# Optimization experiments

Measured on AMD Instinct MI355X. Metric: run time of the kernel, lower is better.

The kernel has to match this reference:

```python
import jax, jax.numpy as jnp
import numpy as np

B, T, OBS, ACT, H, OUT, NLAYERS = 4096, 50, 64, 16, 256, 64, 5


def setup_inputs() -> dict:
    key = jax.random.key(0)
    ks = jax.random.split(key, 8)
    w = 0.05
    return {
        "trajectory": jax.random.normal(ks[0], (B, T, OBS), dtype=jnp.float32),
        "actions": jax.random.normal(ks[1], (B, T, ACT), dtype=jnp.float32),
        "Wi": jax.random.normal(ks[2], (OBS + ACT, 4 * H), dtype=jnp.float32) * w,
        "Wh": jax.random.normal(ks[3], (H, 4 * H), dtype=jnp.float32) * w,
        "bh": jnp.zeros((4 * H,), dtype=jnp.float32),
        "mlp_W": jax.random.normal(ks[4], (NLAYERS, H, H), dtype=jnp.float32) * w,
        "mlp_b": jnp.zeros((NLAYERS, H), dtype=jnp.float32),
        "Wout": jax.random.normal(ks[5], (H, OUT), dtype=jnp.float32) * w,
        "bout": jnp.zeros((OUT,), dtype=jnp.float32),
    }


def reference(trajectory, actions, Wi, Wh, bh, mlp_W, mlp_b, Wout, bout):
    # Features extractor = flatten (identity for 1D sensor obs); preprocess is identity for Box.
    x = jnp.concatenate([trajectory, actions], axis=-1)  # [B, T, OBS+ACT]
    xs = jnp.swapaxes(x, 0, 1)  # [T, B, D] for scan over time

    hdim = Wh.shape[0]
    c0 = jnp.zeros((x.shape[0], hdim), dtype=x.dtype)
    h0 = jnp.zeros((x.shape[0], hdim), dtype=x.dtype)

    def step(carry, xt):
        c, h = carry
        z = xt @ Wi + h @ Wh + bh  # [B, 4H]
        zi, zf, zg, zo = jnp.split(z, 4, axis=-1)
        i = jax.nn.sigmoid(zi)
        f = jax.nn.sigmoid(zf)
        g = jax.nn.silu(zg)  # activation_fn=nn.silu
        o = jax.nn.sigmoid(zo)
        c_new = f * c + i * g
        h_new = o * jax.nn.silu(c_new)
        return (c_new, h_new), None

    (c, h), _ = jax.lax.scan(step, (c0, h0), xs)

    out = h
    for k in range(mlp_W.shape[0]):
        out = jax.nn.silu(out @ mlp_W[k] + mlp_b[k])
    pred = out @ Wout + bout
    return pred
```

## Files before the change

kernel.cpp:

```cpp
#include <hip/hip_runtime.h>
#include <hip/hip_fp16.h>


typedef _Float16 h8 __attribute__((ext_vector_type(8)));
typedef _Float16 hv4 __attribute__((ext_vector_type(4)));
typedef float f4 __attribute__((ext_vector_type(4)));

#define NB    4096
#define TSEQ  50
#define DOBS  64
#define DACT  16
#define HD    256
#define DOUT  64
#define NL    5

#define NKT   11
#define AROW  360
#define MTILE 16
#define NWG   (NB / MTILE)
#define NTHR  512

#define WS_MLP   (704 * 512)
#define WS_WOUT  (WS_MLP + 640 * 512)

#define LDS_AS     (MTILE * AROW)
#define LDS_WCOFF  (2 * LDS_AS)
#define WCB        16
#define LDS_HALVES (LDS_WCOFF + 8 * WCB * 512)
#define LDS_BYTES  (LDS_HALVES * 2)
static_assert(LDS_BYTES <= 160 * 1024, "LDS overflow");

#define SB_P     13
#define NSTREAM  52

__device__ __forceinline__ void lds_barrier() {
  asm volatile("s_waitcnt lgkmcnt(0)\n\ts_barrier" ::: "memory");
}

__device__ constexpr int soff(int c) {
  int kt, cbb, g;
  if (c < 20)      { kt = c >> 2;              cbb = 1; g = c & 3; }
  else if (c < 24) { kt = 5;                   cbb = 0; g = c - 20; }
  else if (c < 28) { kt = 5;                   cbb = 1; g = c - 24; }
  else if (c < 44) { kt = 6 + ((c - 28) >> 2); cbb = 1; g = (c - 28) & 3; }
  else if (c < 48) { kt = 10;                  cbb = 0; g = c - 44; }
  else             { kt = 10;                  cbb = 1; g = c - 48; }
  return ((g * 16 + cbb) * NKT + kt) * 512;
}

__global__ void __launch_bounds__(256) repack_kernel(
    const float* __restrict__ Wi, const float* __restrict__ Wh,
    const float* __restrict__ mlpW, const float* __restrict__ Wout,
    _Float16* __restrict__ wsW)
{
  const int gt  = blockIdx.x * 256 + threadIdx.x;
  const int gb  = gt >> 6;
  const int l   = gt & 63;
  const int l15 = l & 15;
  const int kb  = (l >> 4) * 8;
  h8 v;
  if (gb < 704) {
    const int nt = gb / NKT, kt = gb - nt * NKT;
    const int n  = nt * 16 + l15;
#pragma unroll
    for (int j = 0; j < 8; ++j) {
      const int k = kt * 32 + kb + j;
      float s = 0.f;
      if (k < 80)       s = Wi[k * 1024 + n];
      else if (k < 336) s = Wh[(k - 80) * 1024 + n];
      v[j] = (_Float16)s;
    }
  } else if (gb < 1344) {
    const int b2 = gb - 704;
    const int L  = b2 >> 7, rr = b2 & 127;
    const int nt = rr >> 3, kt = rr & 7;
    const int n  = nt * 16 + l15;
#pragma unroll
    for (int j = 0; j < 8; ++j) {
      const int k = kt * 32 + kb + j;
      v[j] = (_Float16)mlpW[(size_t)L * 65536 + k * 256 + n];
    }
  } else {
    const int b3 = gb - 1344;
    const int nt = b3 >> 3, kt = b3 & 7;
    const int n  = nt * 16 + l15;
#pragma unroll
    for (int j = 0; j < 8; ++j) {
      const int k = kt * 32 + kb + j;
      v[j] = (_Float16)Wout[k * 64 + n];
    }
  }
  *(h8*)&wsW[(size_t)gb * 512 + l * 8] = v;
}

__global__ void __launch_bounds__(NTHR, 2) lstm_kernel(
    const float* __restrict__ traj, const float* __restrict__ acts,
    const float* __restrict__ bh,   const float* __restrict__ mlpb,
    const float* __restrict__ bout, const _Float16* __restrict__ wsW,
    float* __restrict__ out)
{
  extern __shared__ __align__(16) _Float16 lds[];
  _Float16* As0 = lds;
  _Float16* As1 = lds + LDS_AS;
  _Float16* Wc  = lds + LDS_WCOFF;

  const int tid = threadIdx.x;
  const int w   = tid >> 6;
  const int l   = tid & 63;
  const int l15 = l & 15;
  const int lq  = l >> 4;
  const int rbase = blockIdx.x * MTILE;

  for (int i = tid; i < 2 * LDS_AS; i += NTHR) lds[i] = (_Float16)0.f;

#pragma unroll
  for (int j = 0; j < WCB; ++j) {
    const int g = j & 3, kt = 6 + (j >> 2);
    const h8 v = *(const h8*)&wsW[(size_t)((g * 16 + w * 2) * NKT + kt) * 512 + l * 8];
    *(h8*)&Wc[(w * WCB + j) * 512 + l * 8] = v;
  }

  h8 rw[20];
#pragma unroll
  for (int kt = 0; kt < 5; ++kt)
#pragma unroll
    for (int g = 0; g < 4; ++g)
      rw[kt * 4 + g] = *(const h8*)&wsW[(size_t)((g * 16 + w * 2) * NKT + kt) * 512 + l * 8];

  float c[2][4];
#pragma unroll
  for (int cb = 0; cb < 2; ++cb)
#pragma unroll
    for (int r = 0; r < 4; ++r) c[cb][r] = 0.f;

  float bias[4][2];
#pragma unroll
  for (int g = 0; g < 4; ++g) {
    bias[g][0] = bh[g * 256 + w * 32 + l15];
    bias[g][1] = bh[g * 256 + w * 32 + 16 + l15];
  }

  __syncthreads();

  if (tid < 256) {
    const int r = tid >> 4, q = tid & 15;
    const float4 v = *(const float4*)&traj[(size_t)(rbase + r) * (TSEQ * DOBS) + q * 4];
    hv4 hx = { (_Float16)v.x, (_Float16)v.y, (_Float16)v.z, (_Float16)v.w };
    *(hv4*)&As0[r * AROW + q * 4] = hx;
  } else {
    const int r = (tid - 256) >> 4, q = (tid - 256) & 15;
    As0[r * AROW + 64 + q] = (_Float16)acts[(size_t)(rbase + r) * (TSEQ * DACT) + q];
  }
  __syncthreads();

  unsigned long long wbits = (unsigned long long)(const void*)wsW;

  h8 sb[SB_P];
  {
    const _Float16* wlb0 = wsW + (size_t)(w * 2 * NKT) * 512 + l * 8;
#pragma unroll
    for (int cc = 0; cc < SB_P; ++cc) sb[cc] = *(const h8*)&wlb0[soff(cc)];
  }

  auto step = [&](int t, const _Float16* buf, _Float16* nbuf) {
    asm volatile("" : "+s"(wbits) : : "memory");
    const _Float16* wst = (const _Float16*)wbits;
    const _Float16* wlb = wst + (size_t)(w * 2 * NKT) * 512 + l * 8;

    float4 xv; float xa;
    const bool havex = (t + 1 < TSEQ);
    if (havex) {
      if (tid < 256) {
        const int r = tid >> 4, q = tid & 15;
        xv = *(const float4*)&traj[(size_t)(rbase + r) * (TSEQ * DOBS) + (t + 1) * DOBS + q * 4];
      } else {
        const int r = (tid - 256) >> 4, q = (tid - 256) & 15;
        xa = acts[(size_t)(rbase + r) * (TSEQ * DACT) + (t + 1) * DACT + q];
      }
    }

    f4 acc0[4], acc1[4];
#pragma unroll
    for (int g = 0; g < 4; ++g) {
      acc0[g] = f4{0.f, 0.f, 0.f, 0.f};
      acc1[g] = f4{0.f, 0.f, 0.f, 0.f};
    }

#pragma unroll
    for (int kt = 0; kt < NKT; ++kt) {
      const h8 a0 = *(const h8*)&buf[l15 * AROW + kt * 32 + lq * 8];
#pragma unroll
      for (int g = 0; g < 4; ++g) {
        if (kt < 5) {
          acc0[g] = __builtin_amdgcn_mfma_f32_16x16x32_f16(a0, rw[kt * 4 + g], acc0[g], 0, 0, 0);
        } else if (kt >= 6 && kt <= 9) {
          const h8 bf0 = *(const h8*)&Wc[(w * WCB + (kt - 6) * 4 + g) * 512 + l * 8];
          acc0[g] = __builtin_amdgcn_mfma_f32_16x16x32_f16(a0, bf0, acc0[g], 0, 0, 0);
        } else {
          const int c0 = (kt == 5) ? (20 + g) : (44 + g);
          acc0[g] = __builtin_amdgcn_mfma_f32_16x16x32_f16(a0, sb[c0 % SB_P], acc0[g], 0, 0, 0);
          sb[c0 % SB_P] = *(const h8*)&wlb[soff((c0 + SB_P) % NSTREAM)];
        }

        const int c1 = kt * 4 + g + (kt >= 5 ? 4 : 0) + (kt >= 10 ? 4 : 0);
        acc1[g] = __builtin_amdgcn_mfma_f32_16x16x32_f16(a0, sb[c1 % SB_P], acc1[g], 0, 0, 0);
        sb[c1 % SB_P] = *(const h8*)&wlb[soff((c1 + SB_P) % NSTREAM)];
      }
    }

    const float KE = -1.44269504088896f;
    {
      const int colh = 80 + w * 32 + l15;
#pragma unroll
      for (int r = 0; r < 4; ++r) {
        const float zi = acc0[0][r] + bias[0][0];
        const float zf = acc0[1][r] + bias[1][0];
        const float zg = acc0[2][r] + bias[2][0];
        const float zo = acc0[3][r] + bias[3][0];
        const float ei = __builtin_amdgcn_exp2f(zi * KE);
        const float ef = __builtin_amdgcn_exp2f(zf * KE);
        const float eg = __builtin_amdgcn_exp2f(zg * KE);
        const float eo = __builtin_amdgcn_exp2f(zo * KE);
        const float fg = __builtin_amdgcn_rcpf(1.f + ef);
        const float igg = zg * __builtin_amdgcn_rcpf((1.f + ei) * (1.f + eg));
        const float cn = fg * c[0][r] + igg;
        c[0][r] = cn;
        const float ec = __builtin_amdgcn_exp2f(cn * KE);
        const float hn = cn * __builtin_amdgcn_rcpf((1.f + eo) * (1.f + ec));
        nbuf[(lq * 4 + r) * AROW + colh] = (_Float16)hn;
      }
    }
    {
      const int colh = 80 + w * 32 + 16 + l15;
#pragma unroll
      for (int r = 0; r < 4; ++r) {
        const float zi = acc1[0][r] + bias[0][1];
        const float zf = acc1[1][r] + bias[1][1];
        const float zg = acc1[2][r] + bias[2][1];
        const float zo = acc1[3][r] + bias[3][1];
        const float ei = __builtin_amdgcn_exp2f(zi * KE);
        const float ef = __builtin_amdgcn_exp2f(zf * KE);
        const float eg = __builtin_amdgcn_exp2f(zg * KE);
        const float eo = __builtin_amdgcn_exp2f(zo * KE);
        const float fg = __builtin_amdgcn_rcpf(1.f + ef);
        const float igg = zg * __builtin_amdgcn_rcpf((1.f + ei) * (1.f + eg));
        const float cn = fg * c[1][r] + igg;
        c[1][r] = cn;
        const float ec = __builtin_amdgcn_exp2f(cn * KE);
        const float hn = cn * __builtin_amdgcn_rcpf((1.f + eo) * (1.f + ec));
        nbuf[(lq * 4 + r) * AROW + colh] = (_Float16)hn;
      }
    }

    if (havex) {
      if (tid < 256) {
        const int r = tid >> 4, q = tid & 15;
        hv4 hx = { (_Float16)xv.x, (_Float16)xv.y, (_Float16)xv.z, (_Float16)xv.w };
        *(hv4*)&nbuf[r * AROW + q * 4] = hx;
      } else {
        const int r = (tid - 256) >> 4, q = (tid - 256) & 15;
        nbuf[r * AROW + 64 + q] = (_Float16)xa;
      }
    }
  };

#pragma unroll 1
  for (int t = 0; t < TSEQ; t += 2) {
    step(t, As0, As1);
    lds_barrier();
    step(t + 1, As1, As0);
    lds_barrier();
  }

  for (int i = tid; i < MTILE * HD; i += NTHR) {
    const int r = i >> 8, cc = i & 255;
    As1[r * AROW + cc] = As0[r * AROW + 80 + cc];
  }
  __syncthreads();

#pragma unroll 1
  for (int L = 0; L < NL; ++L) {
    const _Float16* in = (L & 1) ? As0 : As1;
    _Float16*       ob = (L & 1) ? As1 : As0;
    const _Float16* wl = wsW + WS_MLP + (size_t)L * (128 * 512);
    float bcol[2];
    bcol[0] = mlpb[L * HD + w * 32 + l15];
    bcol[1] = mlpb[L * HD + w * 32 + 16 + l15];

    f4 acc[2];
    acc[0] = f4{0.f, 0.f, 0.f, 0.f};
    acc[1] = f4{0.f, 0.f, 0.f, 0.f};
#pragma unroll
    for (int kt = 0; kt < 8; ++kt) {
      const h8 a0 = *(const h8*)&in[l15 * AROW + kt * 32 + lq * 8];
#pragma unroll
      for (int cb = 0; cb < 2; ++cb) {
        const h8 bf = *(const h8*)&wl[(size_t)((w * 2 + cb) * 8 + kt) * 512 + l * 8];
        acc[cb] = __builtin_amdgcn_mfma_f32_16x16x32_f16(a0, bf, acc[cb], 0, 0, 0);
      }
    }
#pragma unroll
    for (int cb = 0; cb < 2; ++cb)
#pragma unroll
      for (int r = 0; r < 4; ++r) {
        const float z = acc[cb][r] + bcol[cb];
        const float ez = __builtin_amdgcn_exp2f(z * -1.44269504088896f);
        ob[(lq * 4 + r) * AROW + w * 32 + cb * 16 + l15] =
            (_Float16)(z * __builtin_amdgcn_rcpf(1.f + ez));
      }
    __syncthreads();
  }

  if (w < 4) {
    const _Float16* wo = wsW + WS_WOUT;
    const float bo = bout[w * 16 + l15];
    f4 acc0 = f4{0.f, 0.f, 0.f, 0.f};
#pragma unroll
    for (int kt = 0; kt < 8; ++kt) {
      const h8 a0 = *(const h8*)&As0[l15 * AROW + kt * 32 + lq * 8];
      const h8 bf = *(const h8*)&wo[(size_t)(w * 8 + kt) * 512 + l * 8];
      acc0 = __builtin_amdgcn_mfma_f32_16x16x32_f16(a0, bf, acc0, 0, 0, 0);
    }
#pragma unroll
    for (int r = 0; r < 4; ++r)
      out[(size_t)(rbase + lq * 4 + r) * DOUT + w * 16 + l15] = acc0[r] + bo;
  }
}

extern "C" void kernel_launch(void* const* d_in, const int* in_sizes, int n_in,
                              void* d_out, int out_size, void* d_ws, size_t ws_size,
                              hipStream_t stream)
{
  const float* traj = (const float*)d_in[0];
  const float* acts = (const float*)d_in[1];
  const float* Wi   = (const float*)d_in[2];
  const float* Wh   = (const float*)d_in[3];
  const float* bh   = (const float*)d_in[4];
  const float* mlpW = (const float*)d_in[5];
  const float* mlpb = (const float*)d_in[6];
  const float* Wout = (const float*)d_in[7];
  const float* bout = (const float*)d_in[8];
  _Float16* wsW = (_Float16*)d_ws;

  (void)hipFuncSetAttribute((const void*)lstm_kernel,
                            hipFuncAttributeMaxDynamicSharedMemorySize, LDS_BYTES);

  repack_kernel<<<344, 256, 0, stream>>>(Wi, Wh, mlpW, Wout, wsW);
  lstm_kernel<<<NWG, NTHR, LDS_BYTES, stream>>>(traj, acts, bh, mlpb, bout, wsW, (float*)d_out);
}
```

Before: 335.0 us.

## Split LSTM gate columns across 16 waves instead of 8 per workgroup

Doubles the workgroup to 1024 threads so each wave owns 16 hidden columns, not 32. This halves the serial MFMA chain per wave in each recurrent timestep. Weight residency is rebalanced to fit: K-tiles 0-2 in registers, 3-4 in LDS, 5-10 streamed from global with a shorter prefetch ring. Total LDS use is about the same, but more waves now compete for register and global bandwidth.

```diff
diff --git a/kernel.cpp b/kernel.cpp
--- a/kernel.cpp
+++ b/kernel.cpp
@@ -18,34 +18,27 @@
 #define AROW  360
 #define MTILE 16
 #define NWG   (NB / MTILE)
-#define NTHR  512
+#define NTHR  1024
 
 #define WS_MLP   (704 * 512)
 #define WS_WOUT  (WS_MLP + 640 * 512)
 
 #define LDS_AS     (MTILE * AROW)
 #define LDS_WCOFF  (2 * LDS_AS)
-#define WCB        16
-#define LDS_HALVES (LDS_WCOFF + 8 * WCB * 512)
+#define WCB        8
+#define LDS_HALVES (LDS_WCOFF + 16 * WCB * 512)
 #define LDS_BYTES  (LDS_HALVES * 2)
 static_assert(LDS_BYTES <= 160 * 1024, "LDS overflow");
 
-#define SB_P     13
-#define NSTREAM  52
+#define SB_P     6
+#define NSTREAM  24
 
 __device__ __forceinline__ void lds_barrier() {
   asm volatile("s_waitcnt lgkmcnt(0)\n\ts_barrier" ::: "memory");
 }
 
 __device__ constexpr int soff(int c) {
-  int kt, cbb, g;
-  if (c < 20)      { kt = c >> 2;              cbb = 1; g = c & 3; }
-  else if (c < 24) { kt = 5;                   cbb = 0; g = c - 20; }
-  else if (c < 28) { kt = 5;                   cbb = 1; g = c - 24; }
-  else if (c < 44) { kt = 6 + ((c - 28) >> 2); cbb = 1; g = (c - 28) & 3; }
-  else if (c < 48) { kt = 10;                  cbb = 0; g = c - 44; }
-  else             { kt = 10;                  cbb = 1; g = c - 48; }
-  return ((g * 16 + cbb) * NKT + kt) * 512;
+  return (((c & 3) * 16) * NKT + 5 + (c >> 2)) * 512;
 }
 
 __global__ void __launch_bounds__(256) repack_kernel(
@@ -93,7 +86,7 @@
   *(h8*)&wsW[(size_t)gb * 512 + l * 8] = v;
 }
 
-__global__ void __launch_bounds__(NTHR, 2) lstm_kernel(
+__global__ void __launch_bounds__(NTHR, 4) lstm_kernel(
     const float* __restrict__ traj, const float* __restrict__ acts,
     const float* __restrict__ bh,   const float* __restrict__ mlpb,
     const float* __restrict__ bout, const _Float16* __restrict__ wsW,
@@ -115,30 +108,25 @@
 
 #pragma unroll
   for (int j = 0; j < WCB; ++j) {
-    const int g = j & 3, kt = 6 + (j >> 2);
-    const h8 v = *(const h8*)&wsW[(size_t)((g * 16 + w * 2) * NKT + kt) * 512 + l * 8];
+    const int g = j & 3, kt = 3 + (j >> 2);
+    const h8 v = *(const h8*)&wsW[(size_t)((g * 16 + w) * NKT + kt) * 512 + l * 8];
     *(h8*)&Wc[(w * WCB + j) * 512 + l * 8] = v;
   }
 
-  h8 rw[20];
-#pragma unroll
-  for (int kt = 0; kt < 5; ++kt)
+  h8 rw[12];
+#pragma unroll
+  for (int kt = 0; kt < 3; ++kt)
 #pragma unroll
     for (int g = 0; g < 4; ++g)
-      rw[kt * 4 + g] = *(const h8*)&wsW[(size_t)((g * 16 + w * 2) * NKT + kt) * 512 + l * 8];
-
-  float c[2][4];
-#pragma unroll
-  for (int cb = 0; cb < 2; ++cb)
-#pragma unroll
-    for (int r = 0; r < 4; ++r) c[cb][r] = 0.f;
-
-  float bias[4][2];
-#pragma unroll
-  for (int g = 0; g < 4; ++g) {
-    bias[g][0] = bh[g * 256 + w * 32 + l15];
-    bias[g][1] = bh[g * 256 + w * 32 + 16 + l15];
-  }
+      rw[kt * 4 + g] = *(const h8*)&wsW[(size_t)((g * 16 + w) * NKT + kt) * 512 + l * 8];
+
+  float c[4];
+#pragma unroll
+  for (int r = 0; r < 4; ++r) c[r] = 0.f;
+
+  float bias[4];
+#pragma unroll
+  for (int g = 0; g < 4; ++g) bias[g] = bh[g * 256 + w * 16 + l15];
 
   __syncthreads();
 
@@ -147,7 +135,7 @@
     const float4 v = *(const float4*)&traj[(size_t)(rbase + r) * (TSEQ * DOBS) + q * 4];
     hv4 hx = { (_Float16)v.x, (_Float16)v.y, (_Float16)v.z, (_Float16)v.w };
     *(hv4*)&As0[r * AROW + q * 4] = hx;
-  } else {
+  } else if (tid < 512) {
     const int r = (tid - 256) >> 4, q = (tid - 256) & 15;
     As0[r * AROW + 64 + q] = (_Float16)acts[(size_t)(rbase + r) * (TSEQ * DACT) + q];
   }
@@ -157,7 +145,7 @@
 
   h8 sb[SB_P];
   {
-    const _Float16* wlb0 = wsW + (size_t)(w * 2 * NKT) * 512 + l * 8;
+    const _Float16* wlb0 = wsW + (size_t)(w * NKT) * 512 + l * 8;
 #pragma unroll
     for (int cc = 0; cc < SB_P; ++cc) sb[cc] = *(const h8*)&wlb0[soff(cc)];
   }
@@ -165,7 +153,7 @@
   auto step = [&](int t, const _Float16* buf, _Float16* nbuf) {
     asm volatile("" : "+s"(wbits) : : "memory");
     const _Float16* wst = (const _Float16*)wbits;
-    const _Float16* wlb = wst + (size_t)(w * 2 * NKT) * 512 + l * 8;
+    const _Float16* wlb = wst + (size_t)(w * NKT) * 512 + l * 8;
 
     float4 xv; float xa;
     const bool havex = (t + 1 < TSEQ);
@@ -173,79 +161,51 @@
       if (tid < 256) {
         const int r = tid >> 4, q = tid & 15;
         xv = *(const float4*)&traj[(size_t)(rbase + r) * (TSEQ * DOBS) + (t + 1) * DOBS + q * 4];
-      } else {
+      } else if (tid < 512) {
         const int r = (tid - 256) >> 4, q = (tid - 256) & 15;
         xa = acts[(size_t)(rbase + r) * (TSEQ * DACT) + (t + 1) * DACT + q];
       }
     }
 
-    f4 acc0[4], acc1[4];
-#pragma unroll
-    for (int g = 0; g < 4; ++g) {
-      acc0[g] = f4{0.f, 0.f, 0.f, 0.f};
-      acc1[g] = f4{0.f, 0.f, 0.f, 0.f};
-    }
+    f4 acc[4];
+#pragma unroll
+    for (int g = 0; g < 4; ++g) acc[g] = f4{0.f, 0.f, 0.f, 0.f};
 
 #pragma unroll
     for (int kt = 0; kt < NKT; ++kt) {
       const h8 a0 = *(const h8*)&buf[l15 * AROW + kt * 32 + lq * 8];
 #pragma unroll
       for (int g = 0; g < 4; ++g) {
-        if (kt < 5) {
-          acc0[g] = __builtin_amdgcn_mfma_f32_16x16x32_f16(a0, rw[kt * 4 + g], acc0[g], 0, 0, 0);
-        } else if (kt >= 6 && kt <= 9) {
-          const h8 bf0 = *(const h8*)&Wc[(w * WCB + (kt - 6) * 4 + g) * 512 + l * 8];
-          acc0[g] = __builtin_amdgcn_mfma_f32_16x16x32_f16(a0, bf0, acc0[g], 0, 0, 0);
+        if (kt < 3) {
+          acc[g] = __builtin_amdgcn_mfma_f32_16x16x32_f16(a0, rw[kt * 4 + g], acc[g], 0, 0, 0);
+        } else if (kt < 5) {
+          const h8 bf = *(const h8*)&Wc[(w * WCB + (kt - 3) * 4 + g) * 512 + l * 8];
+          acc[g] = __builtin_amdgcn_mfma_f32_16x16x32_f16(a0, bf, acc[g], 0, 0, 0);
         } else {
-          const int c0 = (kt == 5) ? (20 + g) : (44 + g);
-          acc0[g] = __builtin_amdgcn_mfma_f32_16x16x32_f16(a0, sb[c0 % SB_P], acc0[g], 0, 0, 0);
-          sb[c0 % SB_P] = *(const h8*)&wlb[soff((c0 + SB_P) % NSTREAM)];
+          const int cc = (kt - 5) * 4 + g;
+          acc[g] = __builtin_amdgcn_mfma_f32_16x16x32_f16(a0, sb[cc % SB_P], acc[g], 0, 0, 0);
+          sb[cc % SB_P] = *(const h8*)&wlb[soff((cc + SB_P) % NSTREAM)];
         }
-
-        const int c1 = kt * 4 + g + (kt >= 5 ? 4 : 0) + (kt >= 10 ? 4 : 0);
-        acc1[g] = __builtin_amdgcn_mfma_f32_16x16x32_f16(a0, sb[c1 % SB_P], acc1[g], 0, 0, 0);
-        sb[c1 % SB_P] = *(const h8*)&wlb[soff((c1 + SB_P) % NSTREAM)];
       }
     }
 
     const float KE = -1.44269504088896f;
     {
-      const int colh = 80 + w * 32 + l15;
+      const int colh = 80 + w * 16 + l15;
 #pragma unroll
       for (int r = 0; r < 4; ++r) {
-        const float zi = acc0[0][r] + bias[0][0];
-        const float zf = acc0[1][r] + bias[1][0];
-        const float zg = acc0[2][r] + bias[2][0];
-        const float zo = acc0[3][r] + bias[3][0];
+        const float zi = acc[0][r] + bias[0];
+        const float zf = acc[1][r] + bias[1];
+        const float zg = acc[2][r] + bias[2];
+        const float zo = acc[3][r] + bias[3];
         const float ei = __builtin_amdgcn_exp2f(zi * KE);
         const float ef = __builtin_amdgcn_exp2f(zf * KE);
         const float eg = __builtin_amdgcn_exp2f(zg * KE);
         const float eo = __builtin_amdgcn_exp2f(zo * KE);
         const float fg = __builtin_amdgcn_rcpf(1.f + ef);
         const float igg = zg * __builtin_amdgcn_rcpf((1.f + ei) * (1.f + eg));
-        const float cn = fg * c[0][r] + igg;
-        c[0][r] = cn;
-        const float ec = __builtin_amdgcn_exp2f(cn * KE);
-        const float hn = cn * __builtin_amdgcn_rcpf((1.f + eo) * (1.f + ec));
-        nbuf[(lq * 4 + r) * AROW + colh] = (_Float16)hn;
-      }
-    }
-    {
-      const int colh = 80 + w * 32 + 16 + l15;
-#pragma unroll
-      for (int r = 0; r < 4; ++r) {
-        const float zi = acc1[0][r] + bias[0][1];
-        const float zf = acc1[1][r] + bias[1][1];
-        const float zg = acc1[2][r] + bias[2][1];
-        const float zo = acc1[3][r] + bias[3][1];
-        const float ei = __builtin_amdgcn_exp2f(zi * KE);
-        const float ef = __builtin_amdgcn_exp2f(zf * KE);
-        const float eg = __builtin_amdgcn_exp2f(zg * KE);
-        const float eo = __builtin_amdgcn_exp2f(zo * KE);
-        const float fg = __builtin_amdgcn_rcpf(1.f + ef);
-        const float igg = zg * __builtin_amdgcn_rcpf((1.f + ei) * (1.f + eg));
-        const float cn = fg * c[1][r] + igg;
-        c[1][r] = cn;
+        const float cn = fg * c[r] + igg;
+        c[r] = cn;
         const float ec = __builtin_amdgcn_exp2f(cn * KE);
         const float hn = cn * __builtin_amdgcn_rcpf((1.f + eo) * (1.f + ec));
         nbuf[(lq * 4 + r) * AROW + colh] = (_Float16)hn;
@@ -257,7 +217,7 @@
         const int r = tid >> 4, q = tid & 15;
         hv4 hx = { (_Float16)xv.x, (_Float16)xv.y, (_Float16)xv.z, (_Float16)xv.w };
         *(hv4*)&nbuf[r * AROW + q * 4] = hx;
-      } else {
+      } else if (tid < 512) {
         const int r = (tid - 256) >> 4, q = (tid - 256) & 15;
         nbuf[r * AROW + 64 + q] = (_Float16)xa;
       }
@@ -283,47 +243,38 @@
     const _Float16* in = (L & 1) ? As0 : As1;
     _Float16*       ob = (L & 1) ? As1 : As0;
     const _Float16* wl = wsW + WS_MLP + (size_t)L * (128 * 512);
-    float bcol[2];
-    bcol[0] = mlpb[L * HD + w * 32 + l15];
-    bcol[1] = mlpb[L * HD + w * 32 + 16 + l15];
-
-    f4 acc[2];
-    acc[0] = f4{0.f, 0.f, 0.f, 0.f};
-    acc[1] = f4{0.f, 0.f, 0.f, 0.f};
+    const float bcol = mlpb[L * HD + w * 16 + l15];
+
+    f4 acc = f4{0.f, 0.f, 0.f, 0.f};
 #pragma unroll
     for (int kt = 0; kt < 8; ++kt) {
       const h8 a0 = *(const h8*)&in[l15 * AROW + kt * 32 + lq * 8];
-#pragma unroll
-      for (int cb = 0; cb < 2; ++cb) {
-        const h8 bf = *(const h8*)&wl[(size_t)((w * 2 + cb) * 8 + kt) * 512 + l * 8];
-        acc[cb] = __builtin_amdgcn_mfma_f32_16x16x32_f16(a0, bf, acc[cb], 0, 0, 0);
-      }
-    }
-#pragma unroll
-    for (int cb = 0; cb < 2; ++cb)
-#pragma unroll
-      for (int r = 0; r < 4; ++r) {
-        const float z = acc[cb][r] + bcol[cb];
-        const float ez = __builtin_amdgcn_exp2f(z * -1.44269504088896f);
-        ob[(lq * 4 + r) * AROW + w * 32 + cb * 16 + l15] =
-            (_Float16)(z * __builtin_amdgcn_rcpf(1.f + ez));
-      }
+      const h8 bf = *(const h8*)&wl[(size_t)(w * 8 + kt) * 512 + l * 8];
+      acc = __builtin_amdgcn_mfma_f32_16x16x32_f16(a0, bf, acc, 0, 0, 0);
+    }
+#pragma unroll
+    for (int r = 0; r < 4; ++r) {
+      const float z = acc[r] + bcol;
+      const float ez = __builtin_amdgcn_exp2f(z * -1.44269504088896f);
+      ob[(lq * 4 + r) * AROW + w * 16 + l15] =
+          (_Float16)(z * __builtin_amdgcn_rcpf(1.f + ez));
+    }
     __syncthreads();
   }
 
   if (w < 4) {
     const _Float16* wo = wsW + WS_WOUT;
     const float bo = bout[w * 16 + l15];
-    f4 acc0 = f4{0.f, 0.f, 0.f, 0.f};
+    f4 acc = f4{0.f, 0.f, 0.f, 0.f};
 #pragma unroll
     for (int kt = 0; kt < 8; ++kt) {
       const h8 a0 = *(const h8*)&As0[l15 * AROW + kt * 32 + lq * 8];
       const h8 bf = *(const h8*)&wo[(size_t)(w * 8 + kt) * 512 + l * 8];
-      acc0 = __builtin_amdgcn_mfma_f32_16x16x32_f16(a0, bf, acc0, 0, 0, 0);
+      acc = __builtin_amdgcn_mfma_f32_16x16x32_f16(a0, bf, acc, 0, 0, 0);
     }
 #pragma unroll
     for (int r = 0; r < 4; ++r)
-      out[(size_t)(rbase + lq * 4 + r) * DOUT + w * 16 + l15] = acc0[r] + bo;
+      out[(size_t)(rbase + lq * 4 + r) * DOUT + w * 16 + l15] = acc[r] + bo;
   }
 }
 
```

Result: slower. 417.7 us (+24.7%).

## Process 32 batch rows per workgroup to reuse each weight fragment twice

Applied to the files above, without the earlier changes.

Doubles the batch tile per workgroup from 16 to 32 rows, so every loaded Wh/Wi fragment feeds two MFMAs (one per 16-row half). The weight staging is rebalanced to fit: fewer register-resident k-tiles, fewer LDS-cached ones, and a longer, shallower global stream whose offset map is redone to match. The aim is to halve weight traffic per row and halve the workgroup count for the bandwidth-bound recurrent loop. In exchange, accumulator and cell-state registers double and there are only 128 workgroups, which may leave CUs idle and lengthen each step's serial latency.

```diff
diff --git a/kernel.cpp b/kernel.cpp
--- a/kernel.cpp
+++ b/kernel.cpp
@@ -16,7 +16,7 @@
 
 #define NKT   11
 #define AROW  360
-#define MTILE 16
+#define MTILE 32
 #define NWG   (NB / MTILE)
 #define NTHR  512
 
@@ -25,27 +25,25 @@
 
 #define LDS_AS     (MTILE * AROW)
 #define LDS_WCOFF  (2 * LDS_AS)
-#define WCB        16
+#define WCB        12
 #define LDS_HALVES (LDS_WCOFF + 8 * WCB * 512)
 #define LDS_BYTES  (LDS_HALVES * 2)
 static_assert(LDS_BYTES <= 160 * 1024, "LDS overflow");
 
-#define SB_P     13
-#define NSTREAM  52
+#define SB_P     6
+#define NSTREAM  60
 
 __device__ __forceinline__ void lds_barrier() {
   asm volatile("s_waitcnt lgkmcnt(0)\n\ts_barrier" ::: "memory");
 }
 
 __device__ constexpr int soff(int c) {
-  int kt, cbb, g;
-  if (c < 20)      { kt = c >> 2;              cbb = 1; g = c & 3; }
-  else if (c < 24) { kt = 5;                   cbb = 0; g = c - 20; }
-  else if (c < 28) { kt = 5;                   cbb = 1; g = c - 24; }
-  else if (c < 44) { kt = 6 + ((c - 28) >> 2); cbb = 1; g = (c - 28) & 3; }
-  else if (c < 48) { kt = 10;                  cbb = 0; g = c - 44; }
-  else             { kt = 10;                  cbb = 1; g = c - 48; }
-  return ((g * 16 + cbb) * NKT + kt) * 512;
+  if (c < 28) { const int g = c & 3, kt = c >> 2; return ((g * 16 + 1) * NKT + kt) * 512; }
+  const int q = c - 28;
+  const int kt = 7 + (q >> 3);
+  const int r = q & 7;
+  const int g = r >> 1, cb = r & 1;
+  return ((g * 16 + cb) * NKT + kt) * 512;
 }
 
 __global__ void __launch_bounds__(256) repack_kernel(
@@ -115,23 +113,25 @@
 
 #pragma unroll
   for (int j = 0; j < WCB; ++j) {
-    const int g = j & 3, kt = 6 + (j >> 2);
+    const int g = j & 3, kt = 4 + (j >> 2);
     const h8 v = *(const h8*)&wsW[(size_t)((g * 16 + w * 2) * NKT + kt) * 512 + l * 8];
     *(h8*)&Wc[(w * WCB + j) * 512 + l * 8] = v;
   }
 
-  h8 rw[20];
-#pragma unroll
-  for (int kt = 0; kt < 5; ++kt)
+  h8 rw[16];
+#pragma unroll
+  for (int kt = 0; kt < 4; ++kt)
 #pragma unroll
     for (int g = 0; g < 4; ++g)
       rw[kt * 4 + g] = *(const h8*)&wsW[(size_t)((g * 16 + w * 2) * NKT + kt) * 512 + l * 8];
 
-  float c[2][4];
+  float c[2][2][4];
 #pragma unroll
   for (int cb = 0; cb < 2; ++cb)
 #pragma unroll
-    for (int r = 0; r < 4; ++r) c[cb][r] = 0.f;
+    for (int m = 0; m < 2; ++m)
+#pragma unroll
+      for (int r = 0; r < 4; ++r) c[cb][m][r] = 0.f;
 
   float bias[4][2];
 #pragma unroll
@@ -142,13 +142,11 @@
 
   __syncthreads();
 
-  if (tid < 256) {
+  {
     const int r = tid >> 4, q = tid & 15;
     const float4 v = *(const float4*)&traj[(size_t)(rbase + r) * (TSEQ * DOBS) + q * 4];
     hv4 hx = { (_Float16)v.x, (_Float16)v.y, (_Float16)v.z, (_Float16)v.w };
     *(hv4*)&As0[r * AROW + q * 4] = hx;
-  } else {
-    const int r = (tid - 256) >> 4, q = (tid - 256) & 15;
     As0[r * AROW + 64 + q] = (_Float16)acts[(size_t)(rbase + r) * (TSEQ * DACT) + q];
   }
   __syncthreads();
@@ -170,97 +168,75 @@
     float4 xv; float xa;
     const bool havex = (t + 1 < TSEQ);
     if (havex) {
-      if (tid < 256) {
-        const int r = tid >> 4, q = tid & 15;
-        xv = *(const float4*)&traj[(size_t)(rbase + r) * (TSEQ * DOBS) + (t + 1) * DOBS + q * 4];
-      } else {
-        const int r = (tid - 256) >> 4, q = (tid - 256) & 15;
-        xa = acts[(size_t)(rbase + r) * (TSEQ * DACT) + (t + 1) * DACT + q];
-      }
-    }
-
-    f4 acc0[4], acc1[4];
-#pragma unroll
-    for (int g = 0; g < 4; ++g) {
-      acc0[g] = f4{0.f, 0.f, 0.f, 0.f};
-      acc1[g] = f4{0.f, 0.f, 0.f, 0.f};
-    }
+      const int r = tid >> 4, q = tid & 15;
+      xv = *(const float4*)&traj[(size_t)(rbase + r) * (TSEQ * DOBS) + (t + 1) * DOBS + q * 4];
+      xa = acts[(size_t)(rbase + r) * (TSEQ * DACT) + (t + 1) * DACT + q];
+    }
+
+    f4 acc[2][2][4];
+#pragma unroll
+    for (int m = 0; m < 2; ++m)
+#pragma unroll
+      for (int cb = 0; cb < 2; ++cb)
+#pragma unroll
+        for (int g = 0; g < 4; ++g) acc[m][cb][g] = f4{0.f, 0.f, 0.f, 0.f};
 
 #pragma unroll
     for (int kt = 0; kt < NKT; ++kt) {
       const h8 a0 = *(const h8*)&buf[l15 * AROW + kt * 32 + lq * 8];
+      const h8 a1 = *(const h8*)&buf[(16 + l15) * AROW + kt * 32 + lq * 8];
 #pragma unroll
       for (int g = 0; g < 4; ++g) {
-        if (kt < 5) {
-          acc0[g] = __builtin_amdgcn_mfma_f32_16x16x32_f16(a0, rw[kt * 4 + g], acc0[g], 0, 0, 0);
-        } else if (kt >= 6 && kt <= 9) {
-          const h8 bf0 = *(const h8*)&Wc[(w * WCB + (kt - 6) * 4 + g) * 512 + l * 8];
-          acc0[g] = __builtin_amdgcn_mfma_f32_16x16x32_f16(a0, bf0, acc0[g], 0, 0, 0);
-        } else {
-          const int c0 = (kt == 5) ? (20 + g) : (44 + g);
-          acc0[g] = __builtin_amdgcn_mfma_f32_16x16x32_f16(a0, sb[c0 % SB_P], acc0[g], 0, 0, 0);
+        h8 bf0;
+        if (kt < 4)      bf0 = rw[kt * 4 + g];
+        else if (kt < 7) bf0 = *(const h8*)&Wc[(w * WCB + (kt - 4) * 4 + g) * 512 + l * 8];
+        else {
+          const int c0 = 28 + (kt - 7) * 8 + g * 2;
+          bf0 = sb[c0 % SB_P];
           sb[c0 % SB_P] = *(const h8*)&wlb[soff((c0 + SB_P) % NSTREAM)];
         }
-
-        const int c1 = kt * 4 + g + (kt >= 5 ? 4 : 0) + (kt >= 10 ? 4 : 0);
-        acc1[g] = __builtin_amdgcn_mfma_f32_16x16x32_f16(a0, sb[c1 % SB_P], acc1[g], 0, 0, 0);
+        acc[0][0][g] = __builtin_amdgcn_mfma_f32_16x16x32_f16(a0, bf0, acc[0][0][g], 0, 0, 0);
+        acc[1][0][g] = __builtin_amdgcn_mfma_f32_16x16x32_f16(a1, bf0, acc[1][0][g], 0, 0, 0);
+
+        const int c1 = (kt < 7) ? (kt * 4 + g) : (29 + (kt - 7) * 8 + g * 2);
+        const h8 bf1 = sb[c1 % SB_P];
         sb[c1 % SB_P] = *(const h8*)&wlb[soff((c1 + SB_P) % NSTREAM)];
+        acc[0][1][g] = __builtin_amdgcn_mfma_f32_16x16x32_f16(a0, bf1, acc[0][1][g], 0, 0, 0);
+        acc[1][1][g] = __builtin_amdgcn_mfma_f32_16x16x32_f16(a1, bf1, acc[1][1][g], 0, 0, 0);
       }
     }
 
     const float KE = -1.44269504088896f;
-    {
-      const int colh = 80 + w * 32 + l15;
-#pragma unroll
-      for (int r = 0; r < 4; ++r) {
-        const float zi = acc0[0][r] + bias[0][0];
-        const float zf = acc0[1][r] + bias[1][0];
-        const float zg = acc0[2][r] + bias[2][0];
-        const float zo = acc0[3][r] + bias[3][0];
-        const float ei = __builtin_amdgcn_exp2f(zi * KE);
-        const float ef = __builtin_amdgcn_exp2f(zf * KE);
-        const float eg = __builtin_amdgcn_exp2f(zg * KE);
-        const float eo = __builtin_amdgcn_exp2f(zo * KE);
-        const float fg = __builtin_amdgcn_rcpf(1.f + ef);
-        const float igg = zg * __builtin_amdgcn_rcpf((1.f + ei) * (1.f + eg));
-        const float cn = fg * c[0][r] + igg;
-        c[0][r] = cn;
-        const float ec = __builtin_amdgcn_exp2f(cn * KE);
-        const float hn = cn * __builtin_amdgcn_rcpf((1.f + eo) * (1.f + ec));
-        nbuf[(lq * 4 + r) * AROW + colh] = (_Float16)hn;
-      }
-    }
-    {
-      const int colh = 80 + w * 32 + 16 + l15;
-#pragma unroll
-      for (int r = 0; r < 4; ++r) {
-        const float zi = acc1[0][r] + bias[0][1];
-        const float zf = acc1[1][r] + bias[1][1];
-        const float zg = acc1[2][r] + bias[2][1];
-        const float zo = acc1[3][r] + bias[3][1];
-        const float ei = __builtin_amdgcn_exp2f(zi * KE);
-        const float ef = __builtin_amdgcn_exp2f(zf * KE);
-        const float eg = __builtin_amdgcn_exp2f(zg * KE);
-        const float eo = __builtin_amdgcn_exp2f(zo * KE);
-        const float fg = __builtin_amdgcn_rcpf(1.f + ef);
-        const float igg = zg * __builtin_amdgcn_rcpf((1.f + ei) * (1.f + eg));
-        const float cn = fg * c[1][r] + igg;
-        c[1][r] = cn;
-        const float ec = __builtin_amdgcn_exp2f(cn * KE);
-        const float hn = cn * __builtin_amdgcn_rcpf((1.f + eo) * (1.f + ec));
-        nbuf[(lq * 4 + r) * AROW + colh] = (_Float16)hn;
-      }
+#pragma unroll
+    for (int cb = 0; cb < 2; ++cb) {
+      const int colh = 80 + w * 32 + cb * 16 + l15;
+#pragma unroll
+      for (int m = 0; m < 2; ++m)
+#pragma unroll
+        for (int r = 0; r < 4; ++r) {
+          const float zi = acc[m][cb][0][r] + bias[0][cb];
+          const float zf = acc[m][cb][1][r] + bias[1][cb];
+          const float zg = acc[m][cb][2][r] + bias[2][cb];
+          const float zo = acc[m][cb][3][r] + bias[3][cb];
+          const float ei = __builtin_amdgcn_exp2f(zi * KE);
+          const float ef = __builtin_amdgcn_exp2f(zf * KE);
+          const float eg = __builtin_amdgcn_exp2f(zg * KE);
+          const float eo = __builtin_amdgcn_exp2f(zo * KE);
+          const float fg = __builtin_amdgcn_rcpf(1.f + ef);
+          const float igg = zg * __builtin_amdgcn_rcpf((1.f + ei) * (1.f + eg));
+          const float cn = fg * c[cb][m][r] + igg;
+          c[cb][m][r] = cn;
+          const float ec = __builtin_amdgcn_exp2f(cn * KE);
+          const float hn = cn * __builtin_amdgcn_rcpf((1.f + eo) * (1.f + ec));
+          nbuf[(m * 16 + lq * 4 + r) * AROW + colh] = (_Float16)hn;
+        }
     }
 
     if (havex) {
-      if (tid < 256) {
-        const int r = tid >> 4, q = tid & 15;
-        hv4 hx = { (_Float16)xv.x, (_Float16)xv.y, (_Float16)xv.z, (_Float16)xv.w };
-        *(hv4*)&nbuf[r * AROW + q * 4] = hx;
-      } else {
-        const int r = (tid - 256) >> 4, q = (tid - 256) & 15;
-        nbuf[r * AROW + 64 + q] = (_Float16)xa;
-      }
+      const int r = tid >> 4, q = tid & 15;
+      hv4 hx = { (_Float16)xv.x, (_Float16)xv.y, (_Float16)xv.z, (_Float16)xv.w };
+      *(hv4*)&nbuf[r * AROW + q * 4] = hx;
+      nbuf[r * AROW + 64 + q] = (_Float16)xa;
     }
   };
 
@@ -287,43 +263,55 @@
     bcol[0] = mlpb[L * HD + w * 32 + l15];
     bcol[1] = mlpb[L * HD + w * 32 + 16 + l15];
 
+    f4 acc[2][2];
+#pragma unroll
+    for (int m = 0; m < 2; ++m)
+#pragma unroll
+      for (int cb = 0; cb < 2; ++cb) acc[m][cb] = f4{0.f, 0.f, 0.f, 0.f};
+#pragma unroll
+    for (int kt = 0; kt < 8; ++kt) {
+      const h8 a0 = *(const h8*)&in[l15 * AROW + kt * 32 + lq * 8];
+      const h8 a1 = *(const h8*)&in[(16 + l15) * AROW + kt * 32 + lq * 8];
+#pragma unroll
+      for (int cb = 0; cb < 2; ++cb) {
+        const h8 bf = *(const h8*)&wl[(size_t)((w * 2 + cb) * 8 + kt) * 512 + l * 8];
+        acc[0][cb] = __builtin_amdgcn_mfma_f32_16x16x32_f16(a0, bf, acc[0][cb], 0, 0, 0);
+        acc[1][cb] = __builtin_amdgcn_mfma_f32_16x16x32_f16(a1, bf, acc[1][cb], 0, 0, 0);
+      }
+    }
+#pragma unroll
+    for (int cb = 0; cb < 2; ++cb)
+#pragma unroll
+      for (int m = 0; m < 2; ++m)
+#pragma unroll
+        for (int r = 0; r < 4; ++r) {
+          const float z = acc[m][cb][r] + bcol[cb];
+          const float ez = __builtin_amdgcn_exp2f(z * -1.44269504088896f);
+          ob[(m * 16 + lq * 4 + r) * AROW + w * 32 + cb * 16 + l15] =
+              (_Float16)(z * __builtin_amdgcn_rcpf(1.f + ez));
+        }
+    __syncthreads();
+  }
+
+  if (w < 4) {
+    const _Float16* wo = wsW + WS_WOUT;
+    const float bo = bout[w * 16 + l15];
     f4 acc[2];
     acc[0] = f4{0.f, 0.f, 0.f, 0.f};
     acc[1] = f4{0.f, 0.f, 0.f, 0.f};
 #pragma unroll
     for (int kt = 0; kt < 8; ++kt) {
-      const h8 a0 = *(const h8*)&in[l15 * AROW + kt * 32 + lq * 8];
-#pragma unroll
-      for (int cb = 0; cb < 2; ++cb) {
-        const h8 bf = *(const h8*)&wl[(size_t)((w * 2 + cb) * 8 + kt) * 512 + l * 8];
-        acc[cb] = __builtin_amdgcn_mfma_f32_16x16x32_f16(a0, bf, acc[cb], 0, 0, 0);
-      }
-    }
-#pragma unroll
-    for (int cb = 0; cb < 2; ++cb)
-#pragma unroll
-      for (int r = 0; r < 4; ++r) {
-        const float z = acc[cb][r] + bcol[cb];
-        const float ez = __builtin_amdgcn_exp2f(z * -1.44269504088896f);
-        ob[(lq * 4 + r) * AROW + w * 32 + cb * 16 + l15] =
-            (_Float16)(z * __builtin_amdgcn_rcpf(1.f + ez));
-      }
-    __syncthreads();
-  }
-
-  if (w < 4) {
-    const _Float16* wo = wsW + WS_WOUT;
-    const float bo = bout[w * 16 + l15];
-    f4 acc0 = f4{0.f, 0.f, 0.f, 0.f};
-#pragma unroll
-    for (int kt = 0; kt < 8; ++kt) {
       const h8 a0 = *(const h8*)&As0[l15 * AROW + kt * 32 + lq * 8];
+      const h8 a1 = *(const h8*)&As0[(16 + l15) * AROW + kt * 32 + lq * 8];
       const h8 bf = *(const h8*)&wo[(size_t)(w * 8 + kt) * 512 + l * 8];
-      acc0 = __builtin_amdgcn_mfma_f32_16x16x32_f16(a0, bf, acc0, 0, 0, 0);
-    }
-#pragma unroll
-    for (int r = 0; r < 4; ++r)
-      out[(size_t)(rbase + lq * 4 + r) * DOUT + w * 16 + l15] = acc0[r] + bo;
+      acc[0] = __builtin_amdgcn_mfma_f32_16x16x32_f16(a0, bf, acc[0], 0, 0, 0);
+      acc[1] = __builtin_amdgcn_mfma_f32_16x16x32_f16(a1, bf, acc[1], 0, 0, 0);
+    }
+#pragma unroll
+    for (int m = 0; m < 2; ++m)
+#pragma unroll
+      for (int r = 0; r < 4; ++r)
+        out[(size_t)(rbase + m * 16 + lq * 4 + r) * DOUT + w * 16 + l15] = acc[m][r] + bo;
   }
 }
 
```

Result: slower. 495.7 us (+48.0%).
